# Kernel tuning notes

Hardware: AMD Instinct MI355X
Metric: run time of the kernel (lower is better)

The kernel has to match this reference:

```python
import jax, jax.numpy as jnp
import numpy as np

TEMP = 0.07  # InfoCNECauchy temperature


def setup_inputs() -> dict:
    key = jax.random.key(0)
    k1, k2 = jax.random.split(key)
    features = jax.random.normal(k1, (8192, 512), dtype=jnp.float32)  # 2N x d, two augmented views
    labels = jax.random.randint(k2, (8192,), 0, 100)  # unused in selfsupervised mode
    return {"features": features, "labels": labels}


def reference(features, labels):
    n2 = features.shape[0]
    n = n2 // 2
    # squared pairwise Euclidean distances (== torch.cdist(...)**2)
    sq = jnp.sum(features * features, axis=1)
    d2 = jnp.maximum(sq[:, None] + sq[None, :] - 2.0 * (features @ features.T), 0.0)
    # Cauchy similarity kernel: 1 / ((dist / t)^2 + 1)
    sim = 1.0 / (d2 / (TEMP * TEMP) + 1.0)
    # selfsupervised mask: row i is positive only with its partner view i^N,
    # so the masked mean-log reduces to log(sim[i, partner(i)])
    idx = jnp.arange(n2)
    partner = jnp.where(idx < n, idx + n, idx - n)
    pos = jnp.mean(jnp.log(sim[idx, partner]))
    # negatives: sum over row excluding the diagonal (sim diag == 1)
    neg = jnp.mean(jnp.log(jnp.sum(sim, axis=1) - jnp.diagonal(sim)))
    return -(pos - neg)
```

## Files before the change

kernel.cpp:

```cpp
#include <hip/hip_runtime.h>


#define N2 8192
#define DIM 512
#define NT 64
#define NTILES (NT * (NT + 1) / 2)
#define T2 0.0049f

typedef float floatx4 __attribute__((ext_vector_type(4)));
typedef __bf16 bf16x8 __attribute__((ext_vector_type(8)));
typedef __bf16 bf16x4 __attribute__((ext_vector_type(4)));

__device__ __forceinline__ void load_to_lds16(const void* g, void* l) {
  auto gp = (const __attribute__((address_space(1))) void*)(reinterpret_cast<uintptr_t>(g));
  auto lp = (__attribute__((address_space(3))) void*)(reinterpret_cast<uintptr_t>(l));
  __builtin_amdgcn_global_load_lds(gp, lp, 16, 0, 0);
}

__global__ __launch_bounds__(256) void prep_kernel(const float* __restrict__ f,
                                                   __bf16* __restrict__ fbf,
                                                   float* __restrict__ sq,
                                                   float* __restrict__ rowsum) {
  const int t = threadIdx.x;
  if (t < 2) rowsum[blockIdx.x * 2 + t] = 0.f;
  const int row = blockIdx.x * 2 + (t >> 7);
  const int ci = (t & 127) * 4;
  const float4 v = *(const float4*)(f + (size_t)row * DIM + ci);
  bf16x4 b;
  b[0] = (__bf16)v.x; b[1] = (__bf16)v.y; b[2] = (__bf16)v.z; b[3] = (__bf16)v.w;
  *(bf16x4*)(fbf + (size_t)row * DIM + ci) = b;
  float s = v.x * v.x + v.y * v.y + v.z * v.z + v.w * v.w;
#pragma unroll
  for (int off = 1; off < 64; off <<= 1) s += __shfl_xor(s, off, 64);
  __shared__ float red[4];
  if ((t & 63) == 0) red[t >> 6] = s;
  __syncthreads();
  if ((t & 127) == 0) sq[row] = red[t >> 6] + red[(t >> 6) + 1];
}

__global__ __launch_bounds__(512, 4) void gemm_kernel(const __bf16* __restrict__ fbf,
                                                      const float* __restrict__ sq,
                                                      float* __restrict__ rowsum,
                                                      float* __restrict__ spart) {
  __shared__ __bf16 aT[128 * 64];
  __shared__ __bf16 bT[128 * 64];

  int by, bx;
  {
    const int x = blockIdx.x & 7;
    int kk = blockIdx.x >> 3;
    int band = x;
    const int n1 = 250 - 16 * x;
    if (kk >= n1) { kk -= n1; band = 15 - x; }
    const int by0 = band * 4;
    int bxx = by0;
    int cnt;
    while (kk >= (cnt = min(4, bxx - by0 + 1))) { kk -= cnt; ++bxx; }
    by = by0 + kk;
    bx = bxx;
  }
  const int brow = by * 128;
  const int bcol = bx * 128;
  const bool diag = (by == bx);

  const int t = threadIdx.x;
  const int lane = t & 63;
  const int w = t >> 6;
  const int wrow = (w >> 2) * 64;
  const int wcol = (w & 3) * 32;
  const int q4 = lane >> 4;
  const int lc = lane & 15;

  floatx4 acc[4][2] = {};

  const int rp = t >> 3;
  const int uu = (t & 7) ^ (rp & 7);
  const int grow = rp * 2 + (uu >> 2);
  const int gofs = (uu & 3) * 8;

  const int up = (((lc & 1) * 4) + q4) ^ (lc >> 1);
  const int rhalf = lc >> 1;

  for (int kt = 0; kt < DIM / 64; ++kt) {
    const int k0 = kt * 64;
#pragma unroll
    for (int ks = 0; ks < 2; ++ks) {
      load_to_lds16(fbf + (size_t)(brow + grow) * DIM + k0 + ks * 32 + gofs,
                    &aT[ks * 4096 + t * 8]);
      load_to_lds16(fbf + (size_t)(bcol + grow) * DIM + k0 + ks * 32 + gofs,
                    &bT[ks * 4096 + t * 8]);
    }
    __syncthreads();
#pragma unroll
    for (int ks = 0; ks < 2; ++ks) {
      bf16x8 af[4], bfr[2];
#pragma unroll
      for (int mr = 0; mr < 4; ++mr)
        af[mr] = *(const bf16x8*)&aT[ks * 4096 + ((wrow >> 1) + mr * 8 + rhalf) * 64 + up * 8];
#pragma unroll
      for (int mc = 0; mc < 2; ++mc)
        bfr[mc] = *(const bf16x8*)&bT[ks * 4096 + ((wcol >> 1) + mc * 8 + rhalf) * 64 + up * 8];
#pragma unroll
      for (int mr = 0; mr < 4; ++mr)
#pragma unroll
        for (int mc = 0; mc < 2; ++mc)
          acc[mr][mc] =
              __builtin_amdgcn_mfma_f32_16x16x32_bf16(af[mr], bfr[mc], acc[mr][mc], 0, 0, 0);
    }
    __syncthreads();
  }

  float sqc[2];
#pragma unroll
  for (int mc = 0; mc < 2; ++mc) sqc[mc] = sq[bcol + wcol + mc * 16 + lc];

  float cs[2] = {0.f, 0.f};

#pragma unroll
  for (int mr = 0; mr < 4; ++mr) {
#pragma unroll
    for (int reg = 0; reg < 4; ++reg) {
      const int r = brow + wrow + mr * 16 + q4 * 4 + reg;
      const float sr = sq[r];
      const int pc = r ^ (N2 / 2);
      float rs = 0.f;
#pragma unroll
      for (int mc = 0; mc < 2; ++mc) {
        const int c = bcol + wcol + mc * 16 + lc;
        const float g = acc[mr][mc][reg];
        const float d2 = fmaxf(sr + sqc[mc] - 2.f * g, 0.f);
        const float s = T2 * __builtin_amdgcn_rcpf(d2 + T2);
        if (c != r) rs += s;
        cs[mc] += s;
        if (c == pc) { spart[r] = s; spart[pc] = s; }
      }
#pragma unroll
      for (int off = 1; off < 16; off <<= 1) rs += __shfl_xor(rs, off, 64);
      if (lc == 0) atomicAdd(&rowsum[r], rs);
    }
  }

  if (!diag) {
#pragma unroll
    for (int mc = 0; mc < 2; ++mc) {
      float v = cs[mc];
      v += __shfl_xor(v, 16, 64);
      v += __shfl_xor(v, 32, 64);
      if (lane < 16) atomicAdd(&rowsum[bcol + wcol + mc * 16 + lane], v);
    }
  }
}

__global__ __launch_bounds__(256) void final_kernel(const float* __restrict__ rowsum,
                                                    const float* __restrict__ spart,
                                                    float* __restrict__ out) {
  const int t = threadIdx.x;
  float a = 0.f;
  for (int r = t; r < N2; r += 256) a += logf(rowsum[r]) - logf(spart[r]);
#pragma unroll
  for (int off = 1; off < 64; off <<= 1) a += __shfl_xor(a, off, 64);
  __shared__ float red[4];
  if ((t & 63) == 0) red[t >> 6] = a;
  __syncthreads();
  if (t == 0) out[0] = (red[0] + red[1] + red[2] + red[3]) * (1.0f / (float)N2);
}

extern "C" void kernel_launch(void* const* d_in, const int* in_sizes, int n_in,
                              void* d_out, int out_size, void* d_ws, size_t ws_size,
                              hipStream_t stream) {
  const float* features = (const float*)d_in[0];
  float* out = (float*)d_out;

  char* ws = (char*)d_ws;
  __bf16* fbf = (__bf16*)ws;
  float* sq = (float*)(ws + (size_t)N2 * DIM * sizeof(__bf16));
  float* rowsum = sq + N2;
  float* spart = rowsum + N2;

  prep_kernel<<<N2 / 2, 256, 0, stream>>>(features, fbf, sq, rowsum);
  gemm_kernel<<<NTILES, 512, 0, stream>>>(fbf, sq, rowsum, spart);
  final_kernel<<<1, 256, 0, stream>>>(rowsum, spart, out);
}
```

Measured before the change: 145.1 us.

## Use 256x256 symmetric tiles with 1024-thread blocks and split tail tiles

Raises the per-block output tile of the symmetric Gram computation from 128x128 to 256x256 using 1024-thread blocks, with each wave computing a 64x64 sub-tile. This halves global/LDS load traffic per output element and reduces atomic rowsum updates. The last tiles are split into 128x128 quadrants run by 512 active threads, to balance the tail and skip the redundant lower quadrant of diagonal tiles. The cost is higher register pressure from 16 accumulators, a larger LDS footprint, fewer resident blocks, and idle half-blocks in the quadrant path.

```diff
diff --git a/kernel.cpp b/kernel.cpp
--- a/kernel.cpp
+++ b/kernel.cpp
@@ -3,8 +3,9 @@
 
 #define N2 8192
 #define DIM 512
-#define NT 64
-#define NTILES (NT * (NT + 1) / 2)
+#define NT2 32
+#define NFULL 512
+#define NGRID 576
 #define T2 0.0049f
 
 typedef float floatx4 __attribute__((ext_vector_type(4)));
@@ -38,115 +39,216 @@
   if ((t & 127) == 0) sq[row] = red[t >> 6] + red[(t >> 6) + 1];
 }
 
-__global__ __launch_bounds__(512, 4) void gemm_kernel(const __bf16* __restrict__ fbf,
-                                                      const float* __restrict__ sq,
-                                                      float* __restrict__ rowsum,
-                                                      float* __restrict__ spart) {
-  __shared__ __bf16 aT[128 * 64];
-  __shared__ __bf16 bT[128 * 64];
-
-  int by, bx;
+__global__ __launch_bounds__(1024, 4) void gemm_kernel(const __bf16* __restrict__ fbf,
+                                                       const float* __restrict__ sq,
+                                                       float* __restrict__ rowsum,
+                                                       float* __restrict__ spart) {
+  __shared__ __bf16 aT[4 * 4096];
+  __shared__ __bf16 bT[4 * 4096];
+
+  int by, bx, quad = -1;
   {
     const int x = blockIdx.x & 7;
-    int kk = blockIdx.x >> 3;
+    int kk;
+    if (blockIdx.x < NFULL) {
+      kk = blockIdx.x >> 3;
+    } else {
+      const int j = (blockIdx.x - NFULL) >> 3;
+      kk = 64 + (j >> 2);
+      quad = j & 3;
+    }
     int band = x;
-    const int n1 = 250 - 16 * x;
+    const int n1 = 63 - 4 * x;
     if (kk >= n1) { kk -= n1; band = 15 - x; }
-    const int by0 = band * 4;
+    const int by0 = band * 2;
     int bxx = by0;
     int cnt;
-    while (kk >= (cnt = min(4, bxx - by0 + 1))) { kk -= cnt; ++bxx; }
+    while (kk >= (cnt = min(2, bxx - by0 + 1))) { kk -= cnt; ++bxx; }
     by = by0 + kk;
     bx = bxx;
   }
-  const int brow = by * 128;
-  const int bcol = bx * 128;
-  const bool diag = (by == bx);
 
   const int t = threadIdx.x;
   const int lane = t & 63;
   const int w = t >> 6;
-  const int wrow = (w >> 2) * 64;
-  const int wcol = (w & 3) * 32;
   const int q4 = lane >> 4;
   const int lc = lane & 15;
-
-  floatx4 acc[4][2] = {};
-
-  const int rp = t >> 3;
-  const int uu = (t & 7) ^ (rp & 7);
-  const int grow = rp * 2 + (uu >> 2);
-  const int gofs = (uu & 3) * 8;
-
   const int up = (((lc & 1) * 4) + q4) ^ (lc >> 1);
   const int rhalf = lc >> 1;
 
-  for (int kt = 0; kt < DIM / 64; ++kt) {
-    const int k0 = kt * 64;
-#pragma unroll
-    for (int ks = 0; ks < 2; ++ks) {
-      load_to_lds16(fbf + (size_t)(brow + grow) * DIM + k0 + ks * 32 + gofs,
-                    &aT[ks * 4096 + t * 8]);
-      load_to_lds16(fbf + (size_t)(bcol + grow) * DIM + k0 + ks * 32 + gofs,
-                    &bT[ks * 4096 + t * 8]);
-    }
-    __syncthreads();
-#pragma unroll
-    for (int ks = 0; ks < 2; ++ks) {
-      bf16x8 af[4], bfr[2];
-#pragma unroll
-      for (int mr = 0; mr < 4; ++mr)
-        af[mr] = *(const bf16x8*)&aT[ks * 4096 + ((wrow >> 1) + mr * 8 + rhalf) * 64 + up * 8];
-#pragma unroll
-      for (int mc = 0; mc < 2; ++mc)
-        bfr[mc] = *(const bf16x8*)&bT[ks * 4096 + ((wcol >> 1) + mc * 8 + rhalf) * 64 + up * 8];
-#pragma unroll
-      for (int mr = 0; mr < 4; ++mr)
-#pragma unroll
-        for (int mc = 0; mc < 2; ++mc)
-          acc[mr][mc] =
-              __builtin_amdgcn_mfma_f32_16x16x32_bf16(af[mr], bfr[mc], acc[mr][mc], 0, 0, 0);
-    }
-    __syncthreads();
-  }
-
-  float sqc[2];
-#pragma unroll
-  for (int mc = 0; mc < 2; ++mc) sqc[mc] = sq[bcol + wcol + mc * 16 + lc];
-
-  float cs[2] = {0.f, 0.f};
-
-#pragma unroll
-  for (int mr = 0; mr < 4; ++mr) {
-#pragma unroll
-    for (int reg = 0; reg < 4; ++reg) {
-      const int r = brow + wrow + mr * 16 + q4 * 4 + reg;
-      const float sr = sq[r];
-      const int pc = r ^ (N2 / 2);
-      float rs = 0.f;
-#pragma unroll
-      for (int mc = 0; mc < 2; ++mc) {
-        const int c = bcol + wcol + mc * 16 + lc;
-        const float g = acc[mr][mc][reg];
-        const float d2 = fmaxf(sr + sqc[mc] - 2.f * g, 0.f);
-        const float s = T2 * __builtin_amdgcn_rcpf(d2 + T2);
-        if (c != r) rs += s;
-        cs[mc] += s;
-        if (c == pc) { spart[r] = s; spart[pc] = s; }
-      }
-#pragma unroll
-      for (int off = 1; off < 16; off <<= 1) rs += __shfl_xor(rs, off, 64);
-      if (lc == 0) atomicAdd(&rowsum[r], rs);
-    }
-  }
-
-  if (!diag) {
-#pragma unroll
-    for (int mc = 0; mc < 2; ++mc) {
-      float v = cs[mc];
-      v += __shfl_xor(v, 16, 64);
-      v += __shfl_xor(v, 32, 64);
-      if (lane < 16) atomicAdd(&rowsum[bcol + wcol + mc * 16 + lane], v);
+  if (quad < 0) {
+    const int brow = by * 256;
+    const int bcol = bx * 256;
+    const bool diag = (brow == bcol);
+    const int wrow = (w >> 2) * 64;
+    const int wcol = (w & 3) * 64;
+    const int rhA = wrow >> 7, rhB = wcol >> 7;
+    const int rbA = (wrow >> 1) & 63, rbB = (wcol >> 1) & 63;
+
+    const int rh = t >> 9;
+    const int s = t & 511;
+    const int rp = s >> 3;
+    const int u = (s & 7) ^ (rp & 7);
+    const int grow = rh * 128 + rp * 2 + (u >> 2);
+    const int gofs = (u & 3) * 8;
+
+    floatx4 acc[4][4] = {};
+
+    for (int kt = 0; kt < DIM / 64; ++kt) {
+      const int k0 = kt * 64;
+#pragma unroll
+      for (int ks = 0; ks < 2; ++ks) {
+        load_to_lds16(fbf + (size_t)(brow + grow) * DIM + k0 + ks * 32 + gofs,
+                      &aT[(rh * 2 + ks) * 4096 + s * 8]);
+        load_to_lds16(fbf + (size_t)(bcol + grow) * DIM + k0 + ks * 32 + gofs,
+                      &bT[(rh * 2 + ks) * 4096 + s * 8]);
+      }
+      __syncthreads();
+#pragma unroll
+      for (int ks = 0; ks < 2; ++ks) {
+        bf16x8 af[4], bfr[4];
+#pragma unroll
+        for (int mr = 0; mr < 4; ++mr)
+          af[mr] = *(const bf16x8*)&aT[(rhA * 2 + ks) * 4096 +
+                                       (rbA + mr * 8 + rhalf) * 64 + up * 8];
+#pragma unroll
+        for (int mc = 0; mc < 4; ++mc)
+          bfr[mc] = *(const bf16x8*)&bT[(rhB * 2 + ks) * 4096 +
+                                        (rbB + mc * 8 + rhalf) * 64 + up * 8];
+#pragma unroll
+        for (int mr = 0; mr < 4; ++mr)
+#pragma unroll
+          for (int mc = 0; mc < 4; ++mc)
+            acc[mr][mc] =
+                __builtin_amdgcn_mfma_f32_16x16x32_bf16(af[mr], bfr[mc], acc[mr][mc], 0, 0, 0);
+      }
+      __syncthreads();
+    }
+
+    float sqc[4];
+#pragma unroll
+    for (int mc = 0; mc < 4; ++mc) sqc[mc] = sq[bcol + wcol + mc * 16 + lc];
+    float cs[4] = {0.f, 0.f, 0.f, 0.f};
+#pragma unroll
+    for (int mr = 0; mr < 4; ++mr) {
+#pragma unroll
+      for (int reg = 0; reg < 4; ++reg) {
+        const int r = brow + wrow + mr * 16 + q4 * 4 + reg;
+        const float sr = sq[r];
+        const int pc = r ^ (N2 / 2);
+        float rs = 0.f;
+#pragma unroll
+        for (int mc = 0; mc < 4; ++mc) {
+          const int c = bcol + wcol + mc * 16 + lc;
+          const float g = acc[mr][mc][reg];
+          const float d2 = fmaxf(sr + sqc[mc] - 2.f * g, 0.f);
+          const float sv = T2 * __builtin_amdgcn_rcpf(d2 + T2);
+          if (c != r) rs += sv;
+          cs[mc] += sv;
+          if (c == pc) { spart[r] = sv; spart[pc] = sv; }
+        }
+#pragma unroll
+        for (int off = 1; off < 16; off <<= 1) rs += __shfl_xor(rs, off, 64);
+        if (lc == 0) atomicAdd(&rowsum[r], rs);
+      }
+    }
+    if (!diag) {
+#pragma unroll
+      for (int mc = 0; mc < 4; ++mc) {
+        float v = cs[mc];
+        v += __shfl_xor(v, 16, 64);
+        v += __shfl_xor(v, 32, 64);
+        if (lane < 16) atomicAdd(&rowsum[bcol + wcol + mc * 16 + lane], v);
+      }
+    }
+  } else {
+    if (by == bx && quad == 2) return;
+    const int brow = by * 256 + (quad >> 1) * 128;
+    const int bcol = bx * 256 + (quad & 1) * 128;
+    const bool diag = (brow == bcol);
+    const int wrow = (w >> 2) * 64;
+    const int wcol = (w & 3) * 32;
+
+    int grow = 0, gofs = 0;
+    if (t < 512) {
+      const int rp = t >> 3;
+      const int u = (t & 7) ^ (rp & 7);
+      grow = rp * 2 + (u >> 2);
+      gofs = (u & 3) * 8;
+    }
+
+    floatx4 acc[4][2] = {};
+
+    for (int kt = 0; kt < DIM / 64; ++kt) {
+      const int k0 = kt * 64;
+      if (t < 512) {
+#pragma unroll
+        for (int ks = 0; ks < 2; ++ks) {
+          load_to_lds16(fbf + (size_t)(brow + grow) * DIM + k0 + ks * 32 + gofs,
+                        &aT[ks * 4096 + t * 8]);
+          load_to_lds16(fbf + (size_t)(bcol + grow) * DIM + k0 + ks * 32 + gofs,
+                        &bT[ks * 4096 + t * 8]);
+        }
+      }
+      __syncthreads();
+      if (w < 8) {
+#pragma unroll
+        for (int ks = 0; ks < 2; ++ks) {
+          bf16x8 af[4], bfr[2];
+#pragma unroll
+          for (int mr = 0; mr < 4; ++mr)
+            af[mr] = *(const bf16x8*)&aT[ks * 4096 + ((wrow >> 1) + mr * 8 + rhalf) * 64 + up * 8];
+#pragma unroll
+          for (int mc = 0; mc < 2; ++mc)
+            bfr[mc] = *(const bf16x8*)&bT[ks * 4096 + ((wcol >> 1) + mc * 8 + rhalf) * 64 + up * 8];
+#pragma unroll
+          for (int mr = 0; mr < 4; ++mr)
+#pragma unroll
+            for (int mc = 0; mc < 2; ++mc)
+              acc[mr][mc] =
+                  __builtin_amdgcn_mfma_f32_16x16x32_bf16(af[mr], bfr[mc], acc[mr][mc], 0, 0, 0);
+        }
+      }
+      __syncthreads();
+    }
+
+    if (w < 8) {
+      float sqc[2];
+#pragma unroll
+      for (int mc = 0; mc < 2; ++mc) sqc[mc] = sq[bcol + wcol + mc * 16 + lc];
+      float cs[2] = {0.f, 0.f};
+#pragma unroll
+      for (int mr = 0; mr < 4; ++mr) {
+#pragma unroll
+        for (int reg = 0; reg < 4; ++reg) {
+          const int r = brow + wrow + mr * 16 + q4 * 4 + reg;
+          const float sr = sq[r];
+          const int pc = r ^ (N2 / 2);
+          float rs = 0.f;
+#pragma unroll
+          for (int mc = 0; mc < 2; ++mc) {
+            const int c = bcol + wcol + mc * 16 + lc;
+            const float g = acc[mr][mc][reg];
+            const float d2 = fmaxf(sr + sqc[mc] - 2.f * g, 0.f);
+            const float sv = T2 * __builtin_amdgcn_rcpf(d2 + T2);
+            if (c != r) rs += sv;
+            cs[mc] += sv;
+            if (c == pc) { spart[r] = sv; spart[pc] = sv; }
+          }
+#pragma unroll
+          for (int off = 1; off < 16; off <<= 1) rs += __shfl_xor(rs, off, 64);
+          if (lc == 0) atomicAdd(&rowsum[r], rs);
+        }
+      }
+      if (!diag) {
+#pragma unroll
+        for (int mc = 0; mc < 2; ++mc) {
+          float v = cs[mc];
+          v += __shfl_xor(v, 16, 64);
+          v += __shfl_xor(v, 32, 64);
+          if (lane < 16) atomicAdd(&rowsum[bcol + wcol + mc * 16 + lane], v);
+        }
+      }
     }
   }
 }
@@ -178,6 +280,6 @@
   float* spart = rowsum + N2;
 
   prep_kernel<<<N2 / 2, 256, 0, stream>>>(features, fbf, sq, rowsum);
-  gemm_kernel<<<NTILES, 512, 0, stream>>>(fbf, sq, rowsum, spart);
+  gemm_kernel<<<NGRID, 1024, 0, stream>>>(fbf, sq, rowsum, spart);
   final_kernel<<<1, 256, 0, stream>>>(rowsum, spart, out);
 }
```

Result: no change. 145.1 us (+0.0%).
